# Optimization experiments

Hardware: AMD Instinct MI355X
Metric: run time of the kernel (lower is better)

Reference implementation:

```python
import jax, jax.numpy as jnp
import numpy as np

N = 100000
F_IN = 128
DIM = 2
E = 3200000


def setup_inputs() -> dict:
    key = jax.random.key(0)
    k1, k2, k3, k4, k5, k6, k7 = jax.random.split(key, 7)
    x = jax.random.normal(k1, (N, F_IN), dtype=jnp.float32)
    edge_index = jax.random.randint(k2, (2, E), 0, N, dtype=jnp.int64)
    edge_attr = jax.random.uniform(k3, (E,), dtype=jnp.float32)
    # GCNConv params: lin weight [F_IN, DIM] (glorot), bias zeros
    conv_w = jax.random.normal(k4, (F_IN, DIM), dtype=jnp.float32) * (1.0 / np.sqrt(F_IN))
    conv_b = jnp.zeros((DIM,), dtype=jnp.float32)
    # TopKPooling score weight [DIM]
    pool_w = jax.random.normal(k5, (DIM,), dtype=jnp.float32)
    # fc: Linear(N*DIM, 1), init normal(0, 0.01), bias 0 (per init_weights)
    fc_w = jax.random.normal(k6, (N * DIM, 1), dtype=jnp.float32) * 0.01
    fc_b = jnp.zeros((1,), dtype=jnp.float32)
    return {"x": x, "edge_index": edge_index, "edge_attr": edge_attr,
            "conv_w": conv_w, "conv_b": conv_b, "pool_w": pool_w,
            "fc_w": fc_w, "fc_b": fc_b}


def reference(x, edge_index, edge_attr, conv_w, conv_b, pool_w, fc_w, fc_b):
    n = x.shape[0]
    row, col = edge_index[0], edge_index[1]
    # --- GCNConv: add self-loops (weight 1), symmetric normalization ---
    loop = jnp.arange(n, dtype=edge_index.dtype)
    row_f = jnp.concatenate([row, loop])
    col_f = jnp.concatenate([col, loop])
    w_f = jnp.concatenate([edge_attr, jnp.ones((n,), dtype=x.dtype)])
    deg = jax.ops.segment_sum(w_f, col_f, num_segments=n)  # [N]
    dinv = jnp.where(deg > 0, jax.lax.rsqrt(deg), 0.0)
    norm = dinv[row_f] * w_f * dinv[col_f]  # [E+N]
    h = x @ conv_w  # [N, DIM] transform-then-propagate
    msg = norm[:, None] * h[row_f]  # [E+N, DIM]
    out = jax.ops.segment_sum(msg, col_f, num_segments=n) + conv_b  # [N, DIM]
    # --- ReLU ---
    out = jax.nn.relu(out)
    # --- TopKPooling with k = N (single graph): score, sort desc, gate ---
    score = jnp.tanh((out @ pool_w) / jnp.linalg.norm(pool_w))  # [N]
    perm = jnp.argsort(-score)
    pooled = out[perm] * score[perm][:, None]  # [N, DIM]
    # --- flatten + fc + sigmoid ---
    flat = pooled.reshape(-1)  # [N*DIM]
    y = jax.nn.sigmoid(flat @ fc_w + fc_b)  # [1]
    return y
```

## Files before the change

kernel.cpp:

```cpp
#include <hip/hip_runtime.h>
#include <math.h>

#define FIN 128
#define W 512
#define S 16
#define MAXG 256
#define CAP 18432u
#define HB 256
#define HT 1024
#define BP 200

__device__ __forceinline__ long long edge_at(const void* p, long long i, unsigned mode) {
  return mode ? ((const long long*)p)[i] : (long long)((const int*)p)[i];
}

__device__ __forceinline__ void atomic_fadd(float* p, float v) {
  __hip_atomic_fetch_add(p, v, __ATOMIC_RELAXED, __HIP_MEMORY_SCOPE_AGENT);
}

__global__ void k_detect(const unsigned* ei, unsigned* mode, float* acc,
                         unsigned* cur, int G) {
  int t = threadIdx.x;
  if (t == 0) {
    unsigned orv = 0;
    for (int i = 1; i < 1024; i += 2) orv |= ei[i];
    *mode = (orv == 0) ? 1u : 0u;
    *acc = 0.0f;
  }
  for (int i = t; i < G; i += 64) cur[i] = (unsigned)i * CAP;
}

__global__ void k_h(const float* __restrict__ x, const float* __restrict__ cw,
                    float* __restrict__ h, int n) {
  int gt = blockIdx.x * blockDim.x + threadIdx.x;
  int node = gt >> 5;
  int sub = gt & 31;
  if (node >= n) return;
  float4 xv = ((const float4*)x)[node * 32 + sub];
  float s0 = xv.x * cw[sub * 8 + 0] + xv.y * cw[sub * 8 + 2] +
             xv.z * cw[sub * 8 + 4] + xv.w * cw[sub * 8 + 6];
  float s1 = xv.x * cw[sub * 8 + 1] + xv.y * cw[sub * 8 + 3] +
             xv.z * cw[sub * 8 + 5] + xv.w * cw[sub * 8 + 7];
  for (int off = 16; off > 0; off >>= 1) {
    s0 += __shfl_down(s0, off, 32);
    s1 += __shfl_down(s1, off, 32);
  }
  if (sub == 0) { h[node * 2] = s0; h[node * 2 + 1] = s1; }
}

__global__ void k_scatter2(const void* ei, const float* __restrict__ attr,
                           long long E, int G, unsigned* cur,
                           uint2* __restrict__ packed,
                           const unsigned* __restrict__ mode) {
  __shared__ unsigned hist[MAXG];
  __shared__ unsigned base[MAXG];
  unsigned m = *mode;
  int t = threadIdx.x;
  if (t < MAXG) hist[t] = 0;
  __syncthreads();
  long long perB = (E + HB - 1) / HB;
  long long b0 = (long long)blockIdx.x * perB;
  long long lim = b0 + perB; if (lim > E) lim = E;
  for (long long e = b0 + t; e < lim; e += HT) {
    int c = (int)edge_at(ei, E + e, m);
    atomicAdd(&hist[c >> 9], 1u);
  }
  __syncthreads();
  if (t < G) base[t] = atomicAdd(&cur[t], hist[t]);
  __syncthreads();
  for (long long e = b0 + t; e < lim; e += HT) {
    int r = (int)edge_at(ei, e, m);
    int c = (int)edge_at(ei, E + e, m);
    float a = attr[e];
    unsigned pos = atomicAdd(&base[c >> 9], 1u);
    packed[pos] = make_uint2(((unsigned)r << 9) | ((unsigned)c & 511u), __float_as_uint(a));
  }
}

__global__ void k_pdeg(const uint2* __restrict__ packed, const unsigned* __restrict__ cur,
                       float* __restrict__ pdeg) {
  __shared__ float sdeg[W];
  int blk = blockIdx.x, t = threadIdx.x;
  int g = blk >> 4, s = blk & (S - 1);
  sdeg[t] = 0.f; sdeg[t + 256] = 0.f;
  __syncthreads();
  unsigned lo = (unsigned)g * CAP, hi = cur[g];
  unsigned len = hi - lo;
  unsigned per = (len + S - 1) / S;
  unsigned mylo = lo + s * per;
  unsigned myhi = mylo + per; if (myhi > hi) myhi = hi;
  for (unsigned b = mylo + t; b < myhi; b += 4 * 256) {
    unsigned k0 = b, k1 = b + 256, k2 = b + 512, k3 = b + 768;
    uint2 p0 = packed[k0];
    uint2 p1 = packed[k1 < myhi ? k1 : b];
    uint2 p2 = packed[k2 < myhi ? k2 : b];
    uint2 p3 = packed[k3 < myhi ? k3 : b];
    atomicAdd(&sdeg[p0.x & (W - 1u)], __uint_as_float(p0.y));
    if (k1 < myhi) atomicAdd(&sdeg[p1.x & (W - 1u)], __uint_as_float(p1.y));
    if (k2 < myhi) atomicAdd(&sdeg[p2.x & (W - 1u)], __uint_as_float(p2.y));
    if (k3 < myhi) atomicAdd(&sdeg[p3.x & (W - 1u)], __uint_as_float(p3.y));
  }
  __syncthreads();
  pdeg[(size_t)blk * W + t] = sdeg[t];
  pdeg[(size_t)blk * W + t + 256] = sdeg[t + 256];
}

__global__ void k_dinv(const float* __restrict__ pdeg, const float* __restrict__ h,
                       float* __restrict__ dinv, float* __restrict__ g, int n) {
  int i = blockIdx.x * blockDim.x + threadIdx.x;
  if (i >= n) return;
  int grp = i >> 9, li = i & (W - 1);
  float d = 1.0f;
#pragma unroll
  for (int s = 0; s < S; ++s) d += pdeg[((size_t)(grp * S + s)) * W + li];
  float di = rsqrtf(d);
  dinv[i] = di;
  g[2 * i]     = di * h[2 * i];
  g[2 * i + 1] = di * h[2 * i + 1];
}

__global__ void k_pmsg(const uint2* __restrict__ packed, const unsigned* __restrict__ cur,
                       const float* __restrict__ gv, float* __restrict__ pacc) {
  __shared__ float sacc[2 * W];
  int blk = blockIdx.x, t = threadIdx.x;
  int g = blk >> 4, s = blk & (S - 1);
#pragma unroll
  for (int i = 0; i < 4; ++i) sacc[t + 256 * i] = 0.f;
  __syncthreads();
  unsigned lo = (unsigned)g * CAP, hi = cur[g];
  unsigned len = hi - lo;
  unsigned per = (len + S - 1) / S;
  unsigned mylo = lo + s * per;
  unsigned myhi = mylo + per; if (myhi > hi) myhi = hi;
  const float2* g2 = (const float2*)gv;
  for (unsigned b = mylo + t; b < myhi; b += 4 * 256) {
    unsigned k1 = b + 256, k2 = b + 512, k3 = b + 768;
    uint2 p0 = packed[b];
    uint2 p1 = packed[k1 < myhi ? k1 : b];
    uint2 p2 = packed[k2 < myhi ? k2 : b];
    uint2 p3 = packed[k3 < myhi ? k3 : b];
    float2 g0 = g2[p0.x >> 9];
    float2 g1 = g2[p1.x >> 9];
    float2 g2v = g2[p2.x >> 9];
    float2 g3 = g2[p3.x >> 9];
    float a0 = __uint_as_float(p0.y), a1 = __uint_as_float(p1.y);
    float a2 = __uint_as_float(p2.y), a3 = __uint_as_float(p3.y);
    unsigned c0 = p0.x & (W - 1u), c1 = p1.x & (W - 1u);
    unsigned c2 = p2.x & (W - 1u), c3 = p3.x & (W - 1u);
    atomicAdd(&sacc[2 * c0],     a0 * g0.x);
    atomicAdd(&sacc[2 * c0 + 1], a0 * g0.y);
    if (k1 < myhi) { atomicAdd(&sacc[2 * c1], a1 * g1.x); atomicAdd(&sacc[2 * c1 + 1], a1 * g1.y); }
    if (k2 < myhi) { atomicAdd(&sacc[2 * c2], a2 * g2v.x); atomicAdd(&sacc[2 * c2 + 1], a2 * g2v.y); }
    if (k3 < myhi) { atomicAdd(&sacc[2 * c3], a3 * g3.x); atomicAdd(&sacc[2 * c3 + 1], a3 * g3.y); }
  }
  __syncthreads();
#pragma unroll
  for (int i = 0; i < 4; ++i) pacc[(size_t)blk * (2 * W) + t + 256 * i] = sacc[t + 256 * i];
}

__global__ void k_gout(const float* __restrict__ pacc, const float* __restrict__ dinv,
                       const float* __restrict__ h, const float* __restrict__ cb,
                       const float* __restrict__ pw, float* __restrict__ out,
                       float* __restrict__ score, unsigned* __restrict__ keys,
                       unsigned* __restrict__ pay, unsigned* __restrict__ table, int n) {
  __shared__ unsigned hist[256];
  int g = blockIdx.x, t = threadIdx.x;
  if (t < 256) hist[t] = 0;
  __syncthreads();
  const float2* p2 = (const float2*)pacc;
  float a0 = 0.f, a1 = 0.f;
#pragma unroll
  for (int s = 0; s < S; ++s) {
    float2 v = p2[(size_t)(g * S + s) * W + t];
    a0 += v.x; a1 += v.y;
  }
  int c = g * W + t;
  if (c < n) {
    float dc = dinv[c];
    float o0 = fmaxf(dc * a0 + dc * dc * h[2 * c]     + cb[0], 0.f);
    float o1 = fmaxf(dc * a1 + dc * dc * h[2 * c + 1] + cb[1], 0.f);
    out[2 * c] = o0; out[2 * c + 1] = o1;
    float pw0 = pw[0], pw1 = pw[1];
    float s = tanhf((o0 * pw0 + o1 * pw1) / sqrtf(pw0 * pw0 + pw1 * pw1));
    score[c] = s;
    unsigned u = __float_as_uint(s);
    unsigned asc = u ^ ((u >> 31) ? 0xFFFFFFFFu : 0x80000000u);
    unsigned key = ~asc;
    keys[c] = key;
    pay[c] = (unsigned)c;
    atomicAdd(&hist[key & 255u], 1u);
  }
  __syncthreads();
  if (t < 256) table[t * BP + g] = hist[t];
}

__global__ void k_rhist(const unsigned* __restrict__ keys, int n, int shift,
                        unsigned* table) {
  __shared__ unsigned hist[256];
  int t = threadIdx.x;
  if (t < 256) hist[t] = 0;
  __syncthreads();
  int g = blockIdx.x * 512 + t;
  if (g < n) atomicAdd(&hist[(keys[g] >> shift) & 255u], 1u);
  __syncthreads();
  if (t < 256) table[t * BP + blockIdx.x] = hist[t];
}

__global__ void k_rscan(unsigned* table, int B) {
  int t = threadIdx.x;
  unsigned* row = table + t * BP;
  uint4* r4 = (uint4*)row;
  int nv = B >> 2;
  unsigned s = 0;
#pragma unroll 8
  for (int i = 0; i < nv; ++i) { uint4 v = r4[i]; s += v.x + v.y + v.z + v.w; }
  for (int i = nv * 4; i < B; ++i) s += row[i];
  int lane = t & 63, w = t >> 6;
  unsigned inc = s;
  for (int off = 1; off < 64; off <<= 1) {
    unsigned nval = __shfl_up(inc, off);
    if (lane >= off) inc += nval;
  }
  __shared__ unsigned wtot[4];
  if (lane == 63) wtot[w] = inc;
  __syncthreads();
  unsigned wpre = 0;
  for (int i = 0; i < w; ++i) wpre += wtot[i];
  unsigned run = wpre + inc - s;
#pragma unroll 8
  for (int i = 0; i < nv; ++i) {
    uint4 v = r4[i]; uint4 o;
    o.x = run; run += v.x; o.y = run; run += v.y;
    o.z = run; run += v.z; o.w = run; run += v.w;
    r4[i] = o;
  }
  for (int i = nv * 4; i < B; ++i) { unsigned v = row[i]; row[i] = run; run += v; }
}

__global__ void k_rscatter(const unsigned* __restrict__ keysIn,
                           const unsigned* __restrict__ payIn, int n, int shift,
                           const unsigned* __restrict__ table,
                           unsigned* keysOut, unsigned* payOut) {
  __shared__ unsigned waveCnt[8 * 256];
  int t = threadIdx.x;
  int lane = t & 63, w = t >> 6;
  for (int q = t; q < 8 * 256; q += 512) waveCnt[q] = 0;
  __syncthreads();
  int g = blockIdx.x * 512 + t;
  bool active = g < n;
  unsigned key = 0, pay = 0, d = 0;
  if (active) { key = keysIn[g]; pay = payIn[g]; d = (key >> shift) & 255u; }
  unsigned long long am = __ballot(active);
  unsigned long long mm = ~0ull;
#pragma unroll
  for (int b = 0; b < 8; ++b) {
    unsigned long long bb = __ballot((d >> b) & 1u);
    mm &= ((d >> b) & 1u) ? bb : ~bb;
  }
  mm &= am;
  int rankw = __popcll(mm & ((1ull << lane) - 1ull));
  if (active && rankw == 0) waveCnt[w * 256 + d] = (unsigned)__popcll(mm);
  __syncthreads();
  if (active) {
    unsigned off = (unsigned)rankw;
    for (int ww = 0; ww < w; ++ww) off += waveCnt[ww * 256 + d];
    unsigned gpos = table[d * BP + blockIdx.x] + off;
    keysOut[gpos] = key;
    payOut[gpos] = pay;
  }
}

__global__ void k_final(const unsigned* __restrict__ perm, const float* __restrict__ out,
                        const float* __restrict__ score, const float* __restrict__ fcw,
                        float* acc, int n) {
  int stride = gridDim.x * blockDim.x;
  float s = 0.f;
  const float2* o2 = (const float2*)out;
  const float2* f2 = (const float2*)fcw;
  for (int j = blockIdx.x * blockDim.x + threadIdx.x; j < n; j += stride) {
    unsigned p = perm[j];
    float2 ov = o2[p];
    float2 fv = f2[j];
    s += score[p] * (ov.x * fv.x + ov.y * fv.y);
  }
  for (int off = 32; off > 0; off >>= 1) s += __shfl_down(s, off);
  if ((threadIdx.x & 63) == 0) atomic_fadd(acc, s);
}

__global__ void k_sigmoid(const float* acc, const float* __restrict__ fcb, float* y) {
  if (threadIdx.x == 0 && blockIdx.x == 0) {
    float z = *acc + fcb[0];
    y[0] = 1.f / (1.f + expf(-z));
  }
}

extern "C" void kernel_launch(void* const* d_in, const int* in_sizes, int n_in,
                              void* d_out, int out_size, void* d_ws, size_t ws_size,
                              hipStream_t stream) {
  const float* x     = (const float*)d_in[0];
  const void*  ei    = d_in[1];
  const float* attr  = (const float*)d_in[2];
  const float* convw = (const float*)d_in[3];
  const float* convb = (const float*)d_in[4];
  const float* poolw = (const float*)d_in[5];
  const float* fcw   = (const float*)d_in[6];
  const float* fcb   = (const float*)d_in[7];
  float* y = (float*)d_out;

  int N = in_sizes[0] / FIN;
  long long E = in_sizes[2];
  int B = (N + 511) / 512;
  int G = (N + W - 1) / W;

  float* ws = (float*)d_ws;
  size_t off = 0;
  uint2* packed  = (uint2*)(ws + off); off += (size_t)2 * G * CAP;
  float* pacc    = ws + off; off += (size_t)2 * G * S * W;
  float* pdeg    = pacc;
  float* h       = ws + off; off += (size_t)2 * N;
  float* dinv    = ws + off; off += (size_t)N;
  float* gv      = ws + off; off += (size_t)2 * N;
  float* outN    = ws + off; off += (size_t)2 * N;
  float* score   = ws + off; off += (size_t)N;
  unsigned* keysA = (unsigned*)(ws + off); off += (size_t)N;
  unsigned* payA  = (unsigned*)(ws + off); off += (size_t)N;
  unsigned* keysB = (unsigned*)(ws + off); off += (size_t)N;
  unsigned* payB  = (unsigned*)(ws + off); off += (size_t)N;
  unsigned* cur   = (unsigned*)(ws + off); off += (size_t)G;
  unsigned* stab  = (unsigned*)(ws + off); off += (size_t)256 * BP;
  float* acc      = ws + off; off += 1;
  unsigned* mode  = (unsigned*)(ws + off); off += 1;

  int nb = (N + 255) / 256;

  k_detect<<<1, 64, 0, stream>>>((const unsigned*)ei, mode, acc, cur, G);
  k_h<<<(N * 32 + 255) / 256, 256, 0, stream>>>(x, convw, h, N);

  k_scatter2<<<HB, HT, 0, stream>>>(ei, attr, E, G, cur, packed, mode);

  k_pdeg<<<G * S, 256, 0, stream>>>(packed, cur, pdeg);
  k_dinv<<<nb, 256, 0, stream>>>(pdeg, h, dinv, gv, N);
  k_pmsg<<<G * S, 256, 0, stream>>>(packed, cur, gv, pacc);
  k_gout<<<G, W, 0, stream>>>(pacc, dinv, h, convb, poolw, outN, score,
                              keysA, payA, stab, N);

  unsigned* ki = keysA; unsigned* pi = payA;
  unsigned* ko = keysB; unsigned* po = payB;
  for (int p = 0; p < 4; ++p) {
    int shift = 8 * p;
    if (p > 0) k_rhist<<<B, 512, 0, stream>>>(ki, N, shift, stab);
    k_rscan<<<1, 256, 0, stream>>>(stab, B);
    k_rscatter<<<B, 512, 0, stream>>>(ki, pi, N, shift, stab, ko, po);
    unsigned* tk = ki; ki = ko; ko = tk;
    unsigned* tp = pi; pi = po; po = tp;
  }

  k_final<<<196, 256, 0, stream>>>(pi, outN, score, fcw, acc, N);
  k_sigmoid<<<1, 64, 0, stream>>>(acc, fcb, y);
}
```

Before: 237.2 us.

## Fuse output, radix sort passes and final reduction into one cooperative kernel

The separate gout, radix histogram, scan, scatter, final dot-product and sigmoid launches are replaced by a single cooperative kernel. It uses grid-wide syncs between radix passes, and each block computes its own prefix from the global count table. The edge scatter loops in k_scatter2 are also unrolled by four to raise memory-level parallelism. This removes about fourteen small kernel launches and their gaps. In exchange it adds grid.sync costs and redundant per-block scans over the full table, and it relies on all 196 blocks being co-resident.

```diff
diff --git a/kernel.cpp b/kernel.cpp
--- a/kernel.cpp
+++ b/kernel.cpp
@@ -1,5 +1,8 @@
 #include <hip/hip_runtime.h>
+#include <hip/hip_cooperative_groups.h>
 #include <math.h>
+
+namespace cg = cooperative_groups;
 
 #define FIN 128
 #define W 512
@@ -61,14 +64,41 @@
   long long perB = (E + HB - 1) / HB;
   long long b0 = (long long)blockIdx.x * perB;
   long long lim = b0 + perB; if (lim > E) lim = E;
-  for (long long e = b0 + t; e < lim; e += HT) {
+  long long e = b0 + t;
+  for (; e + 3LL * HT < lim; e += 4LL * HT) {
+    int c0 = (int)edge_at(ei, E + e, m);
+    int c1 = (int)edge_at(ei, E + e + HT, m);
+    int c2 = (int)edge_at(ei, E + e + 2 * HT, m);
+    int c3 = (int)edge_at(ei, E + e + 3 * HT, m);
+    atomicAdd(&hist[c0 >> 9], 1u);
+    atomicAdd(&hist[c1 >> 9], 1u);
+    atomicAdd(&hist[c2 >> 9], 1u);
+    atomicAdd(&hist[c3 >> 9], 1u);
+  }
+  for (; e < lim; e += HT) {
     int c = (int)edge_at(ei, E + e, m);
     atomicAdd(&hist[c >> 9], 1u);
   }
   __syncthreads();
   if (t < G) base[t] = atomicAdd(&cur[t], hist[t]);
   __syncthreads();
-  for (long long e = b0 + t; e < lim; e += HT) {
+  e = b0 + t;
+  for (; e + 3LL * HT < lim; e += 4LL * HT) {
+    int r0 = (int)edge_at(ei, e, m),          c0 = (int)edge_at(ei, E + e, m);
+    int r1 = (int)edge_at(ei, e + HT, m),     c1 = (int)edge_at(ei, E + e + HT, m);
+    int r2 = (int)edge_at(ei, e + 2 * HT, m), c2 = (int)edge_at(ei, E + e + 2 * HT, m);
+    int r3 = (int)edge_at(ei, e + 3 * HT, m), c3 = (int)edge_at(ei, E + e + 3 * HT, m);
+    float a0 = attr[e], a1 = attr[e + HT], a2 = attr[e + 2 * HT], a3 = attr[e + 3 * HT];
+    unsigned p0 = atomicAdd(&base[c0 >> 9], 1u);
+    packed[p0] = make_uint2(((unsigned)r0 << 9) | ((unsigned)c0 & 511u), __float_as_uint(a0));
+    unsigned p1 = atomicAdd(&base[c1 >> 9], 1u);
+    packed[p1] = make_uint2(((unsigned)r1 << 9) | ((unsigned)c1 & 511u), __float_as_uint(a1));
+    unsigned p2 = atomicAdd(&base[c2 >> 9], 1u);
+    packed[p2] = make_uint2(((unsigned)r2 << 9) | ((unsigned)c2 & 511u), __float_as_uint(a2));
+    unsigned p3 = atomicAdd(&base[c3 >> 9], 1u);
+    packed[p3] = make_uint2(((unsigned)r3 << 9) | ((unsigned)c3 & 511u), __float_as_uint(a3));
+  }
+  for (; e < lim; e += HT) {
     int r = (int)edge_at(ei, e, m);
     int c = (int)edge_at(ei, E + e, m);
     float a = attr[e];
@@ -90,8 +120,8 @@
   unsigned mylo = lo + s * per;
   unsigned myhi = mylo + per; if (myhi > hi) myhi = hi;
   for (unsigned b = mylo + t; b < myhi; b += 4 * 256) {
-    unsigned k0 = b, k1 = b + 256, k2 = b + 512, k3 = b + 768;
-    uint2 p0 = packed[k0];
+    unsigned k1 = b + 256, k2 = b + 512, k3 = b + 768;
+    uint2 p0 = packed[b];
     uint2 p1 = packed[k1 < myhi ? k1 : b];
     uint2 p2 = packed[k2 < myhi ? k2 : b];
     uint2 p3 = packed[k3 < myhi ? k3 : b];
@@ -158,137 +188,131 @@
   for (int i = 0; i < 4; ++i) pacc[(size_t)blk * (2 * W) + t + 256 * i] = sacc[t + 256 * i];
 }
 
-__global__ void k_gout(const float* __restrict__ pacc, const float* __restrict__ dinv,
-                       const float* __restrict__ h, const float* __restrict__ cb,
-                       const float* __restrict__ pw, float* __restrict__ out,
-                       float* __restrict__ score, unsigned* __restrict__ keys,
-                       unsigned* __restrict__ pay, unsigned* __restrict__ table, int n) {
+__global__ void k_sortfused(const float* __restrict__ pacc, const float* __restrict__ dinv,
+                            const float* __restrict__ h, const float* __restrict__ cb,
+                            const float* __restrict__ pw, const float* __restrict__ fcw,
+                            const float* __restrict__ fcb,
+                            float* __restrict__ out, float* __restrict__ score,
+                            unsigned* keysA, unsigned* payA,
+                            unsigned* keysB, unsigned* payB,
+                            unsigned* table, float* acc, float* y, int n) {
+  cg::grid_group grid = cg::this_grid();
   __shared__ unsigned hist[256];
-  int g = blockIdx.x, t = threadIdx.x;
-  if (t < 256) hist[t] = 0;
-  __syncthreads();
+  __shared__ unsigned pfx[256];
+  __shared__ unsigned scn[256];
+  __shared__ unsigned waveCnt[8 * 256];
+  __shared__ float red[8];
+
+  int b = blockIdx.x, t = threadIdx.x;
+  int lane = t & 63, w = t >> 6;
+  int nblk = gridDim.x;
+
   const float2* p2 = (const float2*)pacc;
   float a0 = 0.f, a1 = 0.f;
 #pragma unroll
   for (int s = 0; s < S; ++s) {
-    float2 v = p2[(size_t)(g * S + s) * W + t];
+    float2 v = p2[(size_t)(b * S + s) * W + t];
     a0 += v.x; a1 += v.y;
   }
-  int c = g * W + t;
-  if (c < n) {
+  int c = b * W + t;
+  bool active = c < n;
+  unsigned key = 0u, pay = 0u;
+  if (active) {
     float dc = dinv[c];
     float o0 = fmaxf(dc * a0 + dc * dc * h[2 * c]     + cb[0], 0.f);
     float o1 = fmaxf(dc * a1 + dc * dc * h[2 * c + 1] + cb[1], 0.f);
     out[2 * c] = o0; out[2 * c + 1] = o1;
     float pw0 = pw[0], pw1 = pw[1];
-    float s = tanhf((o0 * pw0 + o1 * pw1) / sqrtf(pw0 * pw0 + pw1 * pw1));
-    score[c] = s;
-    unsigned u = __float_as_uint(s);
+    float sv = tanhf((o0 * pw0 + o1 * pw1) / sqrtf(pw0 * pw0 + pw1 * pw1));
+    score[c] = sv;
+    unsigned u = __float_as_uint(sv);
     unsigned asc = u ^ ((u >> 31) ? 0xFFFFFFFFu : 0x80000000u);
-    unsigned key = ~asc;
-    keys[c] = key;
-    pay[c] = (unsigned)c;
-    atomicAdd(&hist[key & 255u], 1u);
-  }
-  __syncthreads();
-  if (t < 256) table[t * BP + g] = hist[t];
-}
-
-__global__ void k_rhist(const unsigned* __restrict__ keys, int n, int shift,
-                        unsigned* table) {
-  __shared__ unsigned hist[256];
-  int t = threadIdx.x;
-  if (t < 256) hist[t] = 0;
-  __syncthreads();
-  int g = blockIdx.x * 512 + t;
-  if (g < n) atomicAdd(&hist[(keys[g] >> shift) & 255u], 1u);
-  __syncthreads();
-  if (t < 256) table[t * BP + blockIdx.x] = hist[t];
-}
-
-__global__ void k_rscan(unsigned* table, int B) {
-  int t = threadIdx.x;
-  unsigned* row = table + t * BP;
-  uint4* r4 = (uint4*)row;
-  int nv = B >> 2;
-  unsigned s = 0;
-#pragma unroll 8
-  for (int i = 0; i < nv; ++i) { uint4 v = r4[i]; s += v.x + v.y + v.z + v.w; }
-  for (int i = nv * 4; i < B; ++i) s += row[i];
-  int lane = t & 63, w = t >> 6;
-  unsigned inc = s;
-  for (int off = 1; off < 64; off <<= 1) {
-    unsigned nval = __shfl_up(inc, off);
-    if (lane >= off) inc += nval;
-  }
-  __shared__ unsigned wtot[4];
-  if (lane == 63) wtot[w] = inc;
-  __syncthreads();
-  unsigned wpre = 0;
-  for (int i = 0; i < w; ++i) wpre += wtot[i];
-  unsigned run = wpre + inc - s;
-#pragma unroll 8
-  for (int i = 0; i < nv; ++i) {
-    uint4 v = r4[i]; uint4 o;
-    o.x = run; run += v.x; o.y = run; run += v.y;
-    o.z = run; run += v.z; o.w = run; run += v.w;
-    r4[i] = o;
-  }
-  for (int i = nv * 4; i < B; ++i) { unsigned v = row[i]; row[i] = run; run += v; }
-}
-
-__global__ void k_rscatter(const unsigned* __restrict__ keysIn,
-                           const unsigned* __restrict__ payIn, int n, int shift,
-                           const unsigned* __restrict__ table,
-                           unsigned* keysOut, unsigned* payOut) {
-  __shared__ unsigned waveCnt[8 * 256];
-  int t = threadIdx.x;
-  int lane = t & 63, w = t >> 6;
-  for (int q = t; q < 8 * 256; q += 512) waveCnt[q] = 0;
-  __syncthreads();
-  int g = blockIdx.x * 512 + t;
-  bool active = g < n;
-  unsigned key = 0, pay = 0, d = 0;
-  if (active) { key = keysIn[g]; pay = payIn[g]; d = (key >> shift) & 255u; }
-  unsigned long long am = __ballot(active);
-  unsigned long long mm = ~0ull;
-#pragma unroll
-  for (int b = 0; b < 8; ++b) {
-    unsigned long long bb = __ballot((d >> b) & 1u);
-    mm &= ((d >> b) & 1u) ? bb : ~bb;
-  }
-  mm &= am;
-  int rankw = __popcll(mm & ((1ull << lane) - 1ull));
-  if (active && rankw == 0) waveCnt[w * 256 + d] = (unsigned)__popcll(mm);
-  __syncthreads();
-  if (active) {
-    unsigned off = (unsigned)rankw;
-    for (int ww = 0; ww < w; ++ww) off += waveCnt[ww * 256 + d];
-    unsigned gpos = table[d * BP + blockIdx.x] + off;
-    keysOut[gpos] = key;
-    payOut[gpos] = pay;
-  }
-}
-
-__global__ void k_final(const unsigned* __restrict__ perm, const float* __restrict__ out,
-                        const float* __restrict__ score, const float* __restrict__ fcw,
-                        float* acc, int n) {
-  int stride = gridDim.x * blockDim.x;
-  float s = 0.f;
-  const float2* o2 = (const float2*)out;
-  const float2* f2 = (const float2*)fcw;
-  for (int j = blockIdx.x * blockDim.x + threadIdx.x; j < n; j += stride) {
-    unsigned p = perm[j];
-    float2 ov = o2[p];
-    float2 fv = f2[j];
-    s += score[p] * (ov.x * fv.x + ov.y * fv.y);
-  }
-  for (int off = 32; off > 0; off >>= 1) s += __shfl_down(s, off);
-  if ((threadIdx.x & 63) == 0) atomic_fadd(acc, s);
-}
-
-__global__ void k_sigmoid(const float* acc, const float* __restrict__ fcb, float* y) {
-  if (threadIdx.x == 0 && blockIdx.x == 0) {
+    key = ~asc;
+    pay = (unsigned)c;
+  }
+
+  unsigned* ki = keysA; unsigned* pi = payA;
+  unsigned* ko = keysB; unsigned* po = payB;
+  (void)ki; (void)pi;
+
+  for (int p = 0; p < 4; ++p) {
+    int shift = 8 * p;
+    unsigned d = (key >> shift) & 255u;
+    if (t < 256) hist[t] = 0;
+    __syncthreads();
+    if (active) atomicAdd(&hist[d], 1u);
+    __syncthreads();
+    if (t < 256) table[t * BP + b] = hist[t];
+    grid.sync();
+    unsigned rt_total = 0;
+    if (t < 256) {
+      const unsigned* row = table + t * BP;
+      unsigned partial = 0, total = 0;
+#pragma unroll 4
+      for (int i = 0; i < nblk; ++i) {
+        unsigned v = row[i];
+        total += v;
+        partial += (i < b) ? v : 0u;
+      }
+      rt_total = total;
+      scn[t] = total;
+      pfx[t] = partial;
+    }
+    __syncthreads();
+    for (int off = 1; off < 256; off <<= 1) {
+      unsigned add = 0;
+      if (t < 256 && t >= off) add = scn[t - off];
+      __syncthreads();
+      if (t < 256) scn[t] += add;
+      __syncthreads();
+    }
+    if (t < 256) pfx[t] += scn[t] - rt_total;
+    for (int q = t; q < 8 * 256; q += 512) waveCnt[q] = 0;
+    __syncthreads();
+    unsigned long long am = __ballot(active);
+    unsigned long long mm = ~0ull;
+#pragma unroll
+    for (int bb = 0; bb < 8; ++bb) {
+      unsigned long long bl = __ballot((d >> bb) & 1u);
+      mm &= ((d >> bb) & 1u) ? bl : ~bl;
+    }
+    mm &= am;
+    int rankw = __popcll(mm & ((1ull << lane) - 1ull));
+    if (active && rankw == 0) waveCnt[w * 256 + d] = (unsigned)__popcll(mm);
+    __syncthreads();
+    if (active) {
+      unsigned o = (unsigned)rankw;
+      for (int ww = 0; ww < w; ++ww) o += waveCnt[ww * 256 + d];
+      unsigned gpos = pfx[d] + o;
+      ko[gpos] = key;
+      po[gpos] = pay;
+    }
+    grid.sync();
+    if (p < 3) {
+      if (active) { key = ko[c]; pay = po[c]; }
+      unsigned* tk = ki; ki = ko; ko = tk;
+      unsigned* tp = pi; pi = po; po = tp;
+    }
+  }
+
+  float sum = 0.f;
+  if (c < n) {
+    unsigned pp = po[c];
+    float2 ov = ((const float2*)out)[pp];
+    float2 fv = ((const float2*)fcw)[c];
+    sum = score[pp] * (ov.x * fv.x + ov.y * fv.y);
+  }
+  for (int off = 32; off > 0; off >>= 1) sum += __shfl_down(sum, off);
+  if (lane == 0) red[w] = sum;
+  __syncthreads();
+  if (t == 0) {
+    float bs = 0.f;
+#pragma unroll
+    for (int i = 0; i < 8; ++i) bs += red[i];
+    atomic_fadd(acc, bs);
+  }
+  grid.sync();
+  if (b == 0 && t == 0) {
     float z = *acc + fcb[0];
     y[0] = 1.f / (1.f + expf(-z));
   }
@@ -309,7 +333,6 @@
 
   int N = in_sizes[0] / FIN;
   long long E = in_sizes[2];
-  int B = (N + 511) / 512;
   int G = (N + W - 1) / W;
 
   float* ws = (float*)d_ws;
@@ -341,20 +364,19 @@
   k_pdeg<<<G * S, 256, 0, stream>>>(packed, cur, pdeg);
   k_dinv<<<nb, 256, 0, stream>>>(pdeg, h, dinv, gv, N);
   k_pmsg<<<G * S, 256, 0, stream>>>(packed, cur, gv, pacc);
-  k_gout<<<G, W, 0, stream>>>(pacc, dinv, h, convb, poolw, outN, score,
-                              keysA, payA, stab, N);
-
-  unsigned* ki = keysA; unsigned* pi = payA;
-  unsigned* ko = keysB; unsigned* po = payB;
-  for (int p = 0; p < 4; ++p) {
-    int shift = 8 * p;
-    if (p > 0) k_rhist<<<B, 512, 0, stream>>>(ki, N, shift, stab);
-    k_rscan<<<1, 256, 0, stream>>>(stab, B);
-    k_rscatter<<<B, 512, 0, stream>>>(ki, pi, N, shift, stab, ko, po);
-    unsigned* tk = ki; ki = ko; ko = tk;
-    unsigned* tp = pi; pi = po; po = tp;
-  }
-
-  k_final<<<196, 256, 0, stream>>>(pi, outN, score, fcw, acc, N);
-  k_sigmoid<<<1, 64, 0, stream>>>(acc, fcb, y);
-}
+
+  {
+    const float* pacc_c = pacc;
+    const float* dinv_c = dinv;
+    const float* h_c = h;
+    void* args[] = {
+      (void*)&pacc_c, (void*)&dinv_c, (void*)&h_c, (void*)&convb,
+      (void*)&poolw, (void*)&fcw, (void*)&fcb,
+      (void*)&outN, (void*)&score,
+      (void*)&keysA, (void*)&payA, (void*)&keysB, (void*)&payB,
+      (void*)&stab, (void*)&acc, (void*)&y, (void*)&N
+    };
+    hipLaunchCooperativeKernel((void*)k_sortfused, dim3(G), dim3(512),
+                               args, 0, stream);
+  }
+}
```

Result: slower. 423.6 us (+78.6%).
